# Performance work log

Hardware: AMD Instinct MI355X
Metric: run time of the kernel (lower is better)

Reference implementation:

```python
import jax, jax.numpy as jnp
import numpy as np

B, S, E = 4, 4096, 512

def setup_inputs() -> dict:
    key = jax.random.key(0)
    ks = jax.random.split(key, 9)
    scale = 1.0 / np.sqrt(E)  # keep linear weights at realistic init scale
    return {
        "query": jax.random.normal(ks[0], (B, S, E), jnp.float32),
        "key":   jax.random.normal(ks[1], (B, S, E), jnp.float32),
        "value": jax.random.normal(ks[2], (B, S, E), jnp.float32),
        "Wq": jax.random.normal(ks[3], (E, E), jnp.float32) * scale,
        "bq": jax.random.normal(ks[4], (E,), jnp.float32) * scale,
        "Wk": jax.random.normal(ks[5], (E, E), jnp.float32) * scale,
        "bk": jax.random.normal(ks[6], (E,), jnp.float32) * scale,
        "Wv": jax.random.normal(ks[7], (E, E), jnp.float32) * scale,
        "bv": jax.random.normal(ks[8], (E,), jnp.float32) * scale,
    }

def reference(query, key, value, Wq, bq, Wk, bk, Wv, bv):
    # torch Linear: x @ W^T + b
    q = jnp.einsum('bse,oe->bso', query, Wq) + bq
    k = jnp.einsum('bse,oe->bso', key,   Wk) + bk
    v = jnp.einsum('bse,oe->bso', value, Wv) + bv
    # NOTE: module applies NO 1/sqrt(d) scaling (faithful to source)
    scores = jnp.einsum('bqd,bkd->bqk', q, k)          # [B,S,S] materialized
    attn = jax.nn.softmax(scores, axis=-1)
    # dropout is identity in eval / for deterministic reference
    return jnp.einsum('bqk,bkd->bqd', attn, v)         # [B,S,E]
```

## Files before the change

kernel.cpp:

```cpp
#include <hip/hip_runtime.h>

typedef __attribute__((ext_vector_type(8))) _Float16 f16x8;
typedef __attribute__((ext_vector_type(4))) _Float16 f16x4;
typedef __attribute__((ext_vector_type(4))) float f32x4;

#define NB 4
#define NS 4096
#define NE 512

__device__ __forceinline__ f16x8 cvt2(float4 a, float4 b) {
    f16x8 r;
    r[0] = (_Float16)a.x; r[1] = (_Float16)a.y; r[2] = (_Float16)a.z; r[3] = (_Float16)a.w;
    r[4] = (_Float16)b.x; r[5] = (_Float16)b.y; r[6] = (_Float16)b.z; r[7] = (_Float16)b.w;
    return r;
}
__device__ __forceinline__ void gload_lds16(const void* g, void* l) {
    __builtin_amdgcn_global_load_lds(
        (const __attribute__((address_space(1))) void*)g,
        (__attribute__((address_space(3))) void*)l, 16, 0, 0);
}

__global__ __launch_bounds__(256) void proj_kernel(
    const float* __restrict__ Xq, const float* __restrict__ Xk,
    const float* __restrict__ Xv,
    const float* __restrict__ Wq, const float* __restrict__ Wk,
    const float* __restrict__ Wv,
    const float* __restrict__ bq, const float* __restrict__ bk,
    const float* __restrict__ bv,
    _Float16* __restrict__ oq, _Float16* __restrict__ ok,
    _Float16* __restrict__ ovt, int b0)
{
    __shared__ __align__(16) _Float16 As[128 * 32];
    __shared__ __align__(16) _Float16 Bs[128 * 32];
    const int t = threadIdx.x;
    const int w = t >> 6, ln = t & 63;
    const int which = blockIdx.y;
    const float* X    = (which == 0) ? Xq : ((which == 1) ? Xk : Xv);
    const float* W    = (which == 0) ? Wq : ((which == 1) ? Wk : Wv);
    const float* bias = (which == 0) ? bq : ((which == 1) ? bk : bv);

    const int m0 = (blockIdx.x >> 2) * 128;
    const int n0 = (blockIdx.x & 3) * 128;

    const int srow  = t >> 1;
    const int shalf = (t & 1) * 16;
    const float* gA = X + ((size_t)b0 * NS + m0 + srow) * NE + shalf;
    const float* gB = W + (size_t)(n0 + srow) * NE + shalf;
    _Float16* lA = &As[srow * 32 + shalf];
    _Float16* lB = &Bs[srow * 32 + shalf];

    f32x4 acc[4][4] = {};
    const int wm = (w >> 1) * 64, wn = (w & 1) * 64;
    const int lcol = ln & 15, lq = ln >> 4;

    for (int k0 = 0; k0 < NE; k0 += 32) {
        float4 xa0 = *(const float4*)(gA + k0);
        float4 xa1 = *(const float4*)(gA + k0 + 4);
        float4 xa2 = *(const float4*)(gA + k0 + 8);
        float4 xa3 = *(const float4*)(gA + k0 + 12);
        float4 xb0 = *(const float4*)(gB + k0);
        float4 xb1 = *(const float4*)(gB + k0 + 4);
        float4 xb2 = *(const float4*)(gB + k0 + 8);
        float4 xb3 = *(const float4*)(gB + k0 + 12);
        __syncthreads();
        *(f16x8*)lA       = cvt2(xa0, xa1);
        *(f16x8*)(lA + 8) = cvt2(xa2, xa3);
        *(f16x8*)lB       = cvt2(xb0, xb1);
        *(f16x8*)(lB + 8) = cvt2(xb2, xb3);
        __syncthreads();
        f16x8 a[4], b[4];
#pragma unroll
        for (int i = 0; i < 4; i++)
            a[i] = *(const f16x8*)&As[(wm + i * 16 + lcol) * 32 + lq * 8];
#pragma unroll
        for (int j = 0; j < 4; j++)
            b[j] = *(const f16x8*)&Bs[(wn + j * 16 + lcol) * 32 + lq * 8];
#pragma unroll
        for (int i = 0; i < 4; i++)
#pragma unroll
            for (int j = 0; j < 4; j++)
                acc[i][j] = __builtin_amdgcn_mfma_f32_16x16x32_f16(a[i], b[j], acc[i][j], 0, 0, 0);
    }

    if (which == 0) {
#pragma unroll
        for (int j = 0; j < 4; j++) {
            const int col = n0 + wn + j * 16 + lcol;
            const float bb = bias[col];
#pragma unroll
            for (int i = 0; i < 4; i++) {
                const int rbase = m0 + wm + i * 16 + lq * 4;
#pragma unroll
                for (int r = 0; r < 4; r++)
                    oq[(size_t)(rbase + r) * NE + col] = (_Float16)(acc[i][j][r] + bb);
            }
        }
    } else if (which == 1) {
#pragma unroll
        for (int j = 0; j < 4; j++) {
            const int col = n0 + wn + j * 16 + lcol;
            const int cch = col >> 3, clo = col & 7;
            const float bb = bias[col];
#pragma unroll
            for (int i = 0; i < 4; i++) {
                const int rbase = m0 + wm + i * 16 + lq * 4;
#pragma unroll
                for (int r = 0; r < 4; r++) {
                    const int s = rbase + r;
                    ok[(size_t)s * NE + ((cch ^ (s & 7)) << 3) + clo] =
                        (_Float16)(acc[i][j][r] + bb);
                }
            }
        }
    } else {
#pragma unroll
        for (int j = 0; j < 4; j++) {
            const int d = n0 + wn + j * 16 + lcol;
            const float bb = bias[d];
#pragma unroll
            for (int i = 0; i < 4; i++) {
                const int rbase = m0 + wm + i * 16 + lq * 4;
                const int bat = rbase >> 12;
                const int sl  = rbase & 4095;
                const int kc  = sl >> 6;
                const int slot = ((sl >> 3) & 7) ^ (d & 7);
                f16x4 pk;
#pragma unroll
                for (int r = 0; r < 4; r++) pk[r] = (_Float16)(acc[i][j][r] + bb);
                *(f16x4*)&ovt[(((size_t)bat * 64 + kc) * NE + d) * 64 + slot * 8 + (sl & 7)] = pk;
            }
        }
    }
}

__global__ __launch_bounds__(512, 2) void attn_kernel(
    const _Float16* __restrict__ q, const _Float16* __restrict__ ksw,
    const _Float16* __restrict__ vsw, float* __restrict__ out, int b0)
{
    __shared__ __align__(16) _Float16 Kbuf[64 * 512];
    __shared__ __align__(16) _Float16 Vbuf[512 * 64];
    __shared__ __align__(16) _Float16 Pb[64 * 72];
    __shared__ float mpart[2][64];
    __shared__ float lpart[2][64];

    const int t = threadIdx.x, w = t >> 6, ln = t & 63;
    const int lcol = ln & 15, lq = ln >> 4;
    const int rt = w & 3, g = w >> 2;
    const int xm = lcol & 7;
    const int rel = blockIdx.y, babs = b0 + rel;
    const int q0 = blockIdx.x * 64;

    const _Float16* qp = q + ((size_t)rel * NS + q0 + rt * 16 + lcol) * NE + lq * 8;
    f16x8 qf[16];
#pragma unroll
    for (int ks = 0; ks < 16; ks++) qf[ks] = *(const f16x8*)(qp + ks * 32);

    const _Float16* kbase = ksw + (size_t)rel * NS * NE;
    const _Float16* vbase = vsw + (size_t)rel * NS * NE;

    f32x4 oacc[16] = {};
    float m_st[4] = {-1e30f, -1e30f, -1e30f, -1e30f};
    float l_st[4] = {0.f, 0.f, 0.f, 0.f};

    for (int kc = 0; kc < 64; kc++) {
        __syncthreads();
        const _Float16* kc_src = kbase + (size_t)kc * 64 * NE;
        const _Float16* vc_src = vbase + (size_t)kc * NE * 64;
#pragma unroll
        for (int i = 0; i < 8; i++) {
            const int blk = i * 8 + w;
            gload_lds16(kc_src + (size_t)blk * 512 + ln * 8, (_Float16*)Kbuf + blk * 512);
            gload_lds16(vc_src + (size_t)blk * 512 + ln * 8, (_Float16*)Vbuf + blk * 512);
        }
        __syncthreads();

        f32x4 s0 = {}, s1 = {};
#pragma unroll
        for (int ks = 0; ks < 16; ks++) {
            const int ch = ((ks * 4 + lq) ^ xm) * 8;
            f16x8 kb0 = *(const f16x8*)&Kbuf[(g * 32 + lcol) * 512 + ch];
            f16x8 kb1 = *(const f16x8*)&Kbuf[(g * 32 + 16 + lcol) * 512 + ch];
            s0 = __builtin_amdgcn_mfma_f32_16x16x32_f16(qf[ks], kb0, s0, 0, 0, 0);
            s1 = __builtin_amdgcn_mfma_f32_16x16x32_f16(qf[ks], kb1, s1, 0, 0, 0);
        }
#pragma unroll
        for (int r = 0; r < 4; r++) {
            float vmx = fmaxf(s0[r], s1[r]);
#pragma unroll
            for (int msk = 8; msk; msk >>= 1) vmx = fmaxf(vmx, __shfl_xor(vmx, msk, 64));
            if (lcol == 0) mpart[g][rt * 16 + lq * 4 + r] = vmx;
        }
        __syncthreads();

        float alpha[4];
#pragma unroll
        for (int r = 0; r < 4; r++) {
            const int row = rt * 16 + lq * 4 + r;
            float mc = fmaxf(mpart[0][row], mpart[1][row]);
            float mn = fmaxf(m_st[r], mc);
            alpha[r] = __expf(m_st[r] - mn);
            float p0 = __expf(s0[r] - mn);
            float p1 = __expf(s1[r] - mn);
            Pb[row * 72 + g * 32 + lcol]      = (_Float16)p0;
            Pb[row * 72 + g * 32 + 16 + lcol] = (_Float16)p1;
            float sm = p0 + p1;
#pragma unroll
            for (int msk = 8; msk; msk >>= 1) sm += __shfl_xor(sm, msk, 64);
            if (lcol == 0) lpart[g][row] = sm;
            m_st[r] = mn;
        }
        __syncthreads();
#pragma unroll
        for (int r = 0; r < 4; r++) {
            const int row = rt * 16 + lq * 4 + r;
            l_st[r] = l_st[r] * alpha[r] + lpart[0][row] + lpart[1][row];
        }
        bool allone = (alpha[0] == 1.f) & (alpha[1] == 1.f) &
                      (alpha[2] == 1.f) & (alpha[3] == 1.f);
        if (!__all(allone)) {
#pragma unroll
            for (int et = 0; et < 16; et++) {
                oacc[et][0] *= alpha[0]; oacc[et][1] *= alpha[1];
                oacc[et][2] *= alpha[2]; oacc[et][3] *= alpha[3];
            }
        }
        f16x8 pa0 = *(const f16x8*)&Pb[(rt * 16 + lcol) * 72 + lq * 8];
        f16x8 pa1 = *(const f16x8*)&Pb[(rt * 16 + lcol) * 72 + 32 + lq * 8];
#pragma unroll
        for (int et = 0; et < 16; et++) {
            const int e = g * 256 + et * 16 + lcol;
            f16x8 v0 = *(const f16x8*)&Vbuf[e * 64 + ((lq ^ xm) * 8)];
            f16x8 v1 = *(const f16x8*)&Vbuf[e * 64 + (((4 + lq) ^ xm) * 8)];
            oacc[et] = __builtin_amdgcn_mfma_f32_16x16x32_f16(pa0, v0, oacc[et], 0, 0, 0);
            oacc[et] = __builtin_amdgcn_mfma_f32_16x16x32_f16(pa1, v1, oacc[et], 0, 0, 0);
        }
    }

#pragma unroll
    for (int r = 0; r < 4; r++) {
        const float inv = 1.0f / l_st[r];
        const size_t ob = ((size_t)babs * NS + q0 + rt * 16 + lq * 4 + r) * NE + g * 256 + lcol;
#pragma unroll
        for (int et = 0; et < 16; et++)
            out[ob + et * 16] = oacc[et][r] * inv;
    }
}

extern "C" void kernel_launch(void* const* d_in, const int* in_sizes, int n_in,
                              void* d_out, int out_size, void* d_ws, size_t ws_size,
                              hipStream_t stream) {
    const float* query = (const float*)d_in[0];
    const float* key_  = (const float*)d_in[1];
    const float* value = (const float*)d_in[2];
    const float* Wq    = (const float*)d_in[3];
    const float* bq    = (const float*)d_in[4];
    const float* Wk    = (const float*)d_in[5];
    const float* bk    = (const float*)d_in[6];
    const float* Wv    = (const float*)d_in[7];
    const float* bv    = (const float*)d_in[8];

    const size_t per_batch = (size_t)3 * NS * NE * 2;
    int nb_chunk = (int)(ws_size / per_batch);
    if (nb_chunk > NB) nb_chunk = NB;
    if (nb_chunk < 1)  nb_chunk = 1;

    _Float16* qh  = (_Float16*)d_ws;
    _Float16* kh  = qh + (size_t)nb_chunk * NS * NE;
    _Float16* vth = kh + (size_t)nb_chunk * NS * NE;

    for (int b0 = 0; b0 < NB; b0 += nb_chunk) {
        int nb = NB - b0 < nb_chunk ? NB - b0 : nb_chunk;
        proj_kernel<<<dim3(nb * 128, 3, 1), 256, 0, stream>>>(
            query, key_, value, Wq, Wk, Wv, bq, bk, bv, qh, kh, vth, b0);
        attn_kernel<<<dim3(NS / 64, nb, 1), 512, 0, stream>>>(
            qh, kh, vth, (float*)d_out, b0);
    }
}
```

Measured before the change: 517.2 us.

## Double-buffer 32-key K/V tiles in attention with async LDS prefetch

Shrinks the key tile from 64 to 32 and double-buffers K and V in LDS, issuing the next tile's global-to-LDS loads before computing on the current one, with explicit vmcnt waits and fewer barriers per iteration. Each wave group now computes its local max and exp independently, and the partial sums and P fragments are rescaled by the cross-group max, which removes one barrier. It also remaps blocks so each XCD pair works on one batch for L2 locality, changes the V layout to 32-key unswizzled chunks, and raises wave priority around the MFMA loops. The cost is twice as many loop iterations, possible LDS bank conflicts from the unswizzled V reads, and an extra fp16 rescale of P.

Result: slower. 596.0 us (+15.2%).

```diff
diff --git a/kernel.cpp b/kernel.cpp
--- a/kernel.cpp
+++ b/kernel.cpp
@@ -122,12 +122,10 @@
                 const int rbase = m0 + wm + i * 16 + lq * 4;
                 const int bat = rbase >> 12;
                 const int sl  = rbase & 4095;
-                const int kc  = sl >> 6;
-                const int slot = ((sl >> 3) & 7) ^ (d & 7);
                 f16x4 pk;
 #pragma unroll
                 for (int r = 0; r < 4; r++) pk[r] = (_Float16)(acc[i][j][r] + bb);
-                *(f16x4*)&ovt[(((size_t)bat * 64 + kc) * NE + d) * 64 + slot * 8 + (sl & 7)] = pk;
+                *(f16x4*)&ovt[(((size_t)bat * 128 + (sl >> 5)) * NE + d) * 32 + (sl & 31)] = pk;
             }
         }
     }
@@ -137,9 +135,9 @@
     const _Float16* __restrict__ q, const _Float16* __restrict__ ksw,
     const _Float16* __restrict__ vsw, float* __restrict__ out, int b0)
 {
-    __shared__ __align__(16) _Float16 Kbuf[64 * 512];
-    __shared__ __align__(16) _Float16 Vbuf[512 * 64];
-    __shared__ __align__(16) _Float16 Pb[64 * 72];
+    __shared__ __align__(16) _Float16 Kb[2][32 * 512];
+    __shared__ __align__(16) _Float16 Vb[2][512 * 32];
+    __shared__ __align__(16) _Float16 Pb[64 * 40];
     __shared__ float mpart[2][64];
     __shared__ float lpart[2][64];
 
@@ -147,8 +145,16 @@
     const int lcol = ln & 15, lq = ln >> 4;
     const int rt = w & 3, g = w >> 2;
     const int xm = lcol & 7;
-    const int rel = blockIdx.y, babs = b0 + rel;
-    const int q0 = blockIdx.x * 64;
+
+    int qx, rel;
+    if (gridDim.y == 4) {
+        const int id = blockIdx.x + (blockIdx.y << 6);
+        const int xcd = id & 7, slot = id >> 3;
+        rel = xcd >> 1;
+        qx  = ((xcd & 1) << 5) + slot;
+    } else { qx = blockIdx.x; rel = blockIdx.y; }
+    const int babs = b0 + rel;
+    const int q0 = qx * 64;
 
     const _Float16* qp = q + ((size_t)rel * NS + q0 + rt * 16 + lcol) * NE + lq * 8;
     f16x8 qf[16];
@@ -162,61 +168,82 @@
     float m_st[4] = {-1e30f, -1e30f, -1e30f, -1e30f};
     float l_st[4] = {0.f, 0.f, 0.f, 0.f};
 
-    for (int kc = 0; kc < 64; kc++) {
-        __syncthreads();
-        const _Float16* kc_src = kbase + (size_t)kc * 64 * NE;
-        const _Float16* vc_src = vbase + (size_t)kc * NE * 64;
-#pragma unroll
-        for (int i = 0; i < 8; i++) {
+    auto stage = [&](int kc, int pp) {
+        const _Float16* ks_src = kbase + (size_t)kc * 32 * NE;
+        const _Float16* vs_src = vbase + (size_t)kc * NE * 32;
+#pragma unroll
+        for (int i = 0; i < 4; i++) {
             const int blk = i * 8 + w;
-            gload_lds16(kc_src + (size_t)blk * 512 + ln * 8, (_Float16*)Kbuf + blk * 512);
-            gload_lds16(vc_src + (size_t)blk * 512 + ln * 8, (_Float16*)Vbuf + blk * 512);
-        }
-        __syncthreads();
-
-        f32x4 s0 = {}, s1 = {};
+            gload_lds16(ks_src + blk * 512 + ln * 8, &Kb[pp][blk * 512]);
+            gload_lds16(vs_src + blk * 512 + ln * 8, &Vb[pp][blk * 512]);
+        }
+    };
+
+    stage(0, 0);
+
+    for (int kc = 0; kc < NS / 32; kc++) {
+        const int p = kc & 1;
+
+        asm volatile("" ::: "memory");
+        __builtin_amdgcn_s_barrier();
+        asm volatile("" ::: "memory");
+
+        if (kc + 1 < NS / 32) {
+            stage(kc + 1, p ^ 1);
+            asm volatile("s_waitcnt vmcnt(8)" ::: "memory");
+        } else {
+            asm volatile("s_waitcnt vmcnt(0)" ::: "memory");
+        }
+        __builtin_amdgcn_s_barrier();
+        asm volatile("" ::: "memory");
+
+        f32x4 s = {};
+        __builtin_amdgcn_s_setprio(1);
 #pragma unroll
         for (int ks = 0; ks < 16; ks++) {
-            const int ch = ((ks * 4 + lq) ^ xm) * 8;
-            f16x8 kb0 = *(const f16x8*)&Kbuf[(g * 32 + lcol) * 512 + ch];
-            f16x8 kb1 = *(const f16x8*)&Kbuf[(g * 32 + 16 + lcol) * 512 + ch];
-            s0 = __builtin_amdgcn_mfma_f32_16x16x32_f16(qf[ks], kb0, s0, 0, 0, 0);
-            s1 = __builtin_amdgcn_mfma_f32_16x16x32_f16(qf[ks], kb1, s1, 0, 0, 0);
-        }
+            f16x8 kb = *(const f16x8*)&Kb[p][(g * 16 + lcol) * 512 + ((ks * 4 + lq) ^ xm) * 8];
+            s = __builtin_amdgcn_mfma_f32_16x16x32_f16(qf[ks], kb, s, 0, 0, 0);
+        }
+        __builtin_amdgcn_s_setprio(0);
+
+        float pe[4], Mg[4];
 #pragma unroll
         for (int r = 0; r < 4; r++) {
-            float vmx = fmaxf(s0[r], s1[r]);
-#pragma unroll
-            for (int msk = 8; msk; msk >>= 1) vmx = fmaxf(vmx, __shfl_xor(vmx, msk, 64));
-            if (lcol == 0) mpart[g][rt * 16 + lq * 4 + r] = vmx;
-        }
-        __syncthreads();
+            float mx = s[r];
+#pragma unroll
+            for (int msk = 8; msk; msk >>= 1) mx = fmaxf(mx, __shfl_xor(mx, msk, 64));
+            Mg[r] = fmaxf(m_st[r], mx);
+            pe[r] = __expf(s[r] - Mg[r]);
+            Pb[(rt * 16 + lq * 4 + r) * 40 + g * 16 + lcol] = (_Float16)pe[r];
+        }
+#pragma unroll
+        for (int r = 0; r < 4; r++) {
+            float ls = pe[r];
+#pragma unroll
+            for (int msk = 8; msk; msk >>= 1) ls += __shfl_xor(ls, msk, 64);
+            if (lcol == 0) {
+                mpart[g][rt * 16 + lq * 4 + r] = Mg[r];
+                lpart[g][rt * 16 + lq * 4 + r] = ls;
+            }
+        }
+        asm volatile("s_waitcnt lgkmcnt(0)" ::: "memory");
+        __builtin_amdgcn_s_barrier();
+        asm volatile("" ::: "memory");
 
         float alpha[4];
 #pragma unroll
         for (int r = 0; r < 4; r++) {
             const int row = rt * 16 + lq * 4 + r;
-            float mc = fmaxf(mpart[0][row], mpart[1][row]);
-            float mn = fmaxf(m_st[r], mc);
+            const float M0 = mpart[0][row], M1 = mpart[1][row];
+            const float mn = fmaxf(M0, M1);
             alpha[r] = __expf(m_st[r] - mn);
-            float p0 = __expf(s0[r] - mn);
-            float p1 = __expf(s1[r] - mn);
-            Pb[row * 72 + g * 32 + lcol]      = (_Float16)p0;
-            Pb[row * 72 + g * 32 + 16 + lcol] = (_Float16)p1;
-            float sm = p0 + p1;
-#pragma unroll
-            for (int msk = 8; msk; msk >>= 1) sm += __shfl_xor(sm, msk, 64);
-            if (lcol == 0) lpart[g][row] = sm;
+            l_st[r] = l_st[r] * alpha[r]
+                    + __expf(M0 - mn) * lpart[0][row]
+                    + __expf(M1 - mn) * lpart[1][row];
             m_st[r] = mn;
         }
-        __syncthreads();
-#pragma unroll
-        for (int r = 0; r < 4; r++) {
-            const int row = rt * 16 + lq * 4 + r;
-            l_st[r] = l_st[r] * alpha[r] + lpart[0][row] + lpart[1][row];
-        }
-        bool allone = (alpha[0] == 1.f) & (alpha[1] == 1.f) &
-                      (alpha[2] == 1.f) & (alpha[3] == 1.f);
+        const bool allone = (alpha[0] == 1.f) & (alpha[1] == 1.f) &
+                            (alpha[2] == 1.f) & (alpha[3] == 1.f);
         if (!__all(allone)) {
 #pragma unroll
             for (int et = 0; et < 16; et++) {
@@ -224,16 +251,23 @@
                 oacc[et][2] *= alpha[2]; oacc[et][3] *= alpha[3];
             }
         }
-        f16x8 pa0 = *(const f16x8*)&Pb[(rt * 16 + lcol) * 72 + lq * 8];
-        f16x8 pa1 = *(const f16x8*)&Pb[(rt * 16 + lcol) * 72 + 32 + lq * 8];
+
+        const int frow = rt * 16 + lcol;
+        const float F0 = mpart[0][frow], F1 = mpart[1][frow];
+        const float fm = fmaxf(F0, F1);
+        const _Float16 cf = (_Float16)__expf(((lq < 2) ? F0 : F1) - fm);
+        f16x8 pa = *(const f16x8*)&Pb[frow * 40 + lq * 8];
+#pragma unroll
+        for (int j = 0; j < 8; j++) pa[j] *= cf;
+
+        __builtin_amdgcn_s_setprio(1);
 #pragma unroll
         for (int et = 0; et < 16; et++) {
             const int e = g * 256 + et * 16 + lcol;
-            f16x8 v0 = *(const f16x8*)&Vbuf[e * 64 + ((lq ^ xm) * 8)];
-            f16x8 v1 = *(const f16x8*)&Vbuf[e * 64 + (((4 + lq) ^ xm) * 8)];
-            oacc[et] = __builtin_amdgcn_mfma_f32_16x16x32_f16(pa0, v0, oacc[et], 0, 0, 0);
-            oacc[et] = __builtin_amdgcn_mfma_f32_16x16x32_f16(pa1, v1, oacc[et], 0, 0, 0);
-        }
+            f16x8 vf = *(const f16x8*)&Vb[p][e * 32 + lq * 8];
+            oacc[et] = __builtin_amdgcn_mfma_f32_16x16x32_f16(pa, vf, oacc[et], 0, 0, 0);
+        }
+        __builtin_amdgcn_s_setprio(0);
     }
 
 #pragma unroll
```
